# Kernel optimization log

Hardware: AMD Instinct MI355X
Metric: run time of the kernel (lower is better)

The kernel has to match this reference:

```python
import jax, jax.numpy as jnp
import numpy as np

NUM_ANTENNAS = 16
D = 0.5
WAVELENGTH = 1.0
RHO = 0.8


def setup_inputs() -> dict:
    key = jax.random.key(0)
    k = jax.random.split(key, 5)
    return {
        "W": jax.random.normal(k[0], (2_000_000, 2 * NUM_ANTENNAS), dtype=jnp.float32),
        "Hc_real": jax.random.normal(k[1], (4, 8, NUM_ANTENNAS), dtype=jnp.float32),
        "Hc_imag": jax.random.normal(k[2], (4, 8, NUM_ANTENNAS), dtype=jnp.float32),
        "Hs_real": jax.random.normal(k[3], (4, 4, NUM_ANTENNAS), dtype=jnp.float32),
        "Hs_imag": jax.random.normal(k[4], (4, 4, NUM_ANTENNAS), dtype=jnp.float32),
    }


def _estimate_angles(h_real, h_imag):
    """Vectorized version of the per-(b,t) phase-unwrap + OLS slope fit.

    h_real/h_imag: [B, T, N] -> angles [B, T] in degrees.
    """
    n = jnp.arange(NUM_ANTENNAS, dtype=h_real.dtype)
    phases = jnp.arctan2(h_imag, h_real)                      # torch.angle
    pd = jnp.diff(phases, axis=-1)
    pd = (pd + jnp.pi) % (2.0 * jnp.pi) - jnp.pi              # wrap to (-pi, pi]
    zeros = jnp.zeros(phases.shape[:-1] + (1,), phases.dtype)
    unwrapped = jnp.concatenate([zeros, jnp.cumsum(pd, axis=-1)], axis=-1)  # [B,T,N]
    # OLS slope of unwrapped vs n (closed form of solve(XtX, XtY) with X=[n,1])
    n_c = n - n.mean()
    slope = (unwrapped * n_c).sum(-1) / (n_c * n_c).sum()     # [B,T]
    sin_theta = jnp.clip(slope * WAVELENGTH / (2.0 * jnp.pi * D), -1.0, 1.0)
    return -jnp.rad2deg(jnp.arcsin(sin_theta))


def _steering_phase(angles_deg):
    # phase[t, n] = 2*pi*d*n*sin(theta_t)/wavelength  -> [T, N]
    n = jnp.arange(NUM_ANTENNAS, dtype=angles_deg.dtype)
    s = jnp.sin(jnp.deg2rad(angles_deg))
    return 2.0 * jnp.pi * D * s[:, None] * n[None, :] / WAVELENGTH


def reference(W, Hc_real, Hc_imag, Hs_real, Hs_imag):
    user_angles = _estimate_angles(Hc_real, Hc_imag)[0]       # [Tc]
    target_angles = _estimate_angles(Hs_real, Hs_imag)[0]     # [Ts]

    Wr = W[:, :NUM_ANTENNAS]
    Wi = W[:, NUM_ANTENNAS:]

    def gains(phase):  # |w_cplx @ conj(sv).T|, all-real math
        c = jnp.cos(phase)  # [T, N]
        s = jnp.sin(phase)
        re = Wr @ c.T + Wi @ s.T  # [B, T]
        im = Wi @ c.T - Wr @ s.T
        return jnp.sqrt(re * re + im * im)

    user_gains = gains(_steering_phase(user_angles))          # [B, Tc]
    target_gains = gains(_steering_phase(target_angles))      # [B, Ts]

    min_user_gain = user_gains.min(axis=1)
    sum_user_gain = user_gains.sum(axis=1)
    avg_target_gain = target_gains.mean(axis=1)

    comm_loss = -RHO * 2.5 * (min_user_gain + 0.1 * sum_user_gain)
    sens_loss = -(1.0 - RHO) * avg_target_gain
    return jnp.mean(comm_loss + sens_loss)
```

## Files before the change

### kernel.cpp

```cpp
#include <hip/hip_runtime.h>
#include <math.h>

#define NA 16
#define NBEAM 12
#define NUSER 8

#define ACC_OFFSET 1536

__global__ void mtl_angles_kernel(const float* __restrict__ Hc_r, const float* __restrict__ Hc_i,
                                  const float* __restrict__ Hs_r, const float* __restrict__ Hs_i,
                                  float* __restrict__ table, double* __restrict__ acc) {
    int t = threadIdx.x;
    if (t == 0) *acc = 0.0;
    if (t >= NBEAM) return;

    const float* re;
    const float* im;
    if (t < NUSER) { re = Hc_r + t * NA;           im = Hc_i + t * NA; }
    else           { re = Hs_r + (t - NUSER) * NA; im = Hs_i + (t - NUSER) * NA; }

    const float PI_F   = 3.14159265358979323846f;
    const float TWO_PI = 6.28318530717958647692f;

    float ph[NA];
    #pragma unroll
    for (int n = 0; n < NA; ++n) ph[n] = atan2f(im[n], re[n]);

    float unw = 0.f, dotsum = 0.f;
    #pragma unroll
    for (int n = 1; n < NA; ++n) {
        float pd = ph[n] - ph[n - 1];
        float x  = pd + PI_F;
        float m  = fmodf(x, TWO_PI);
        if (m < 0.f) m += TWO_PI;
        pd = m - PI_F;
        unw += pd;
        dotsum += unw * ((float)n - 7.5f);
    }
    float slope = dotsum / 340.0f;
    float sin_theta = slope / PI_F;
    sin_theta = fminf(1.0f, fmaxf(-1.0f, sin_theta));
    float st = -sin_theta;

    #pragma unroll
    for (int n = 0; n < NA; ++n) {
        float phase = PI_F * st * (float)n;
        table[t * 2 * NA + n]      = cosf(phase);
        table[t * 2 * NA + NA + n] = sinf(phase);
    }
}

__device__ __forceinline__ float dot4(float4 a, float4 b) {
    return a.x * b.x + a.y * b.y + a.z * b.z + a.w * b.w;
}

__global__ __launch_bounds__(256, 4) void mtl_gains_kernel(const float* __restrict__ W,
                                                           const float* __restrict__ table,
                                                           double* __restrict__ acc, int rows) {
    __shared__ float sh[NBEAM * 2 * NA];
    for (int i = threadIdx.x; i < NBEAM * 2 * NA; i += blockDim.x) sh[i] = table[i];
    __syncthreads();

    float local = 0.f;
    int tid = blockIdx.x * blockDim.x + threadIdx.x;
    int stride = gridDim.x * blockDim.x;
    #pragma unroll 1
    for (int row = tid; row < rows; row += stride) {
        const float4* wp = (const float4*)(W + (size_t)row * 32);
        float4 w[8];
        #pragma unroll
        for (int i = 0; i < 8; ++i) w[i] = wp[i];

        float minU = 3.4e38f, sumU = 0.f, sumT = 0.f;
        #pragma unroll 1
        for (int j = 0; j < NBEAM; ++j) {
            const float4* tc = (const float4*)(sh + j * 32);
            float re = 0.f, im = 0.f;
            #pragma unroll
            for (int q = 0; q < 4; ++q) {
                float4 c = tc[q], s = tc[q + 4];
                float4 wr = w[q], wi = w[q + 4];
                re += dot4(wr, c) + dot4(wi, s);
                im += dot4(wi, c) - dot4(wr, s);
            }
            float g = sqrtf(re * re + im * im);
            if (j < NUSER) { minU = fminf(minU, g); sumU += g; }
            else           { sumT += g; }
        }
        local += -2.0f * (minU + 0.1f * sumU) - 0.05f * sumT;
    }

    #pragma unroll
    for (int off = 32; off > 0; off >>= 1) local += __shfl_down(local, off);
    __shared__ float wsum[4];
    int lane = threadIdx.x & 63, wid = threadIdx.x >> 6;
    if (lane == 0) wsum[wid] = local;
    __syncthreads();
    if (threadIdx.x == 0) {
        float b = wsum[0] + wsum[1] + wsum[2] + wsum[3];
        atomicAdd(acc, (double)b);
    }
}

__global__ void mtl_finalize_kernel(const double* __restrict__ acc, float* __restrict__ out, int rows) {
    if (threadIdx.x == 0) out[0] = (float)(*acc / (double)rows);
}

extern "C" void kernel_launch(void* const* d_in, const int* in_sizes, int n_in,
                              void* d_out, int out_size, void* d_ws, size_t ws_size,
                              hipStream_t stream) {
    const float* W    = (const float*)d_in[0];
    const float* Hc_r = (const float*)d_in[1];
    const float* Hc_i = (const float*)d_in[2];
    const float* Hs_r = (const float*)d_in[3];
    const float* Hs_i = (const float*)d_in[4];
    float* out = (float*)d_out;

    int rows = in_sizes[0] / (2 * NA);
    float*  table = (float*)d_ws;
    double* acc   = (double*)((char*)d_ws + ACC_OFFSET);

    mtl_angles_kernel<<<1, 64, 0, stream>>>(Hc_r, Hc_i, Hs_r, Hs_i, table, acc);

    const int ROWS_PER_THREAD = 4;
    int blocks = (rows + 256 * ROWS_PER_THREAD - 1) / (256 * ROWS_PER_THREAD);
    mtl_gains_kernel<<<blocks, 256, 0, stream>>>(W, table, acc, rows);

    mtl_finalize_kernel<<<1, 64, 0, stream>>>(acc, out, rows);
}
```

Measured before the change: 366.4 us.

## Stage W tiles through LDS with direct global-to-LDS coalesced loads

Each block now loads a 256-row tile of W into shared memory using global_load_lds so that lanes issue contiguous 16-byte loads, then each thread reads its own row from LDS with a rotated index to spread bank accesses. The grid becomes up to 1024 persistent blocks looping over tiles, with a tail handled by block 0. This targets the strided per-thread row loads of the original, at the cost of two barriers per tile and no overlap between loading and computing.

```diff
diff --git a/kernel.cpp b/kernel.cpp
--- a/kernel.cpp
+++ b/kernel.cpp
@@ -54,45 +54,82 @@
     return a.x * b.x + a.y * b.y + a.z * b.z + a.w * b.w;
 }
 
+__device__ __forceinline__ void load_lds16(const float* g, float* l) {
+    __builtin_amdgcn_global_load_lds(
+        (const __attribute__((address_space(1))) void*)g,
+        (__attribute__((address_space(3))) void*)l, 16, 0, 0);
+}
+
+__device__ __forceinline__ float row_loss(const float4* w, const float* tbs) {
+    float minU = 3.4e38f, sumU = 0.f, sumT = 0.f;
+    #pragma unroll 1
+    for (int j = 0; j < NBEAM; ++j) {
+        const float4* tc = (const float4*)(tbs + j * 32);
+        float re = 0.f, im = 0.f;
+        #pragma unroll
+        for (int q = 0; q < 4; ++q) {
+            float4 c = tc[q], s = tc[q + 4];
+            float4 wr = w[q], wi = w[q + 4];
+            re += dot4(wr, c) + dot4(wi, s);
+            im += dot4(wi, c) - dot4(wr, s);
+        }
+        float g = sqrtf(re * re + im * im);
+        if (j < NUSER) { minU = fminf(minU, g); sumU += g; }
+        else           { sumT += g; }
+    }
+    return -2.0f * (minU + 0.1f * sumU) - 0.05f * sumT;
+}
+
 __global__ __launch_bounds__(256, 4) void mtl_gains_kernel(const float* __restrict__ W,
                                                            const float* __restrict__ table,
                                                            double* __restrict__ acc, int rows) {
-    __shared__ float sh[NBEAM * 2 * NA];
-    for (int i = threadIdx.x; i < NBEAM * 2 * NA; i += blockDim.x) sh[i] = table[i];
+    __shared__ float sh[256 * 32];
+    __shared__ float tbs[NBEAM * 2 * NA];
+    __shared__ float wsum[4];
+
+    for (int i = threadIdx.x; i < NBEAM * 2 * NA; i += blockDim.x) tbs[i] = table[i];
     __syncthreads();
 
+    const int t = threadIdx.x;
+    const int wave_base = (t & 192) * 4;
     float local = 0.f;
-    int tid = blockIdx.x * blockDim.x + threadIdx.x;
-    int stride = gridDim.x * blockDim.x;
+
+    const int ntiles = rows >> 8;
     #pragma unroll 1
-    for (int row = tid; row < rows; row += stride) {
-        const float4* wp = (const float4*)(W + (size_t)row * 32);
+    for (int tile = blockIdx.x; tile < ntiles; tile += gridDim.x) {
+        const float* gW = W + (size_t)tile * 256 * 32;
+        #pragma unroll
+        for (int i = 0; i < 8; ++i) {
+            int k = i * 256 + t;
+            load_lds16(gW + 4 * k, sh + i * 1024 + wave_base);
+        }
+        __syncthreads();
+
+        const float4* myrow = (const float4*)(sh + t * 32);
         float4 w[8];
         #pragma unroll
-        for (int i = 0; i < 8; ++i) w[i] = wp[i];
+        for (int i = 0; i < 8; ++i) {
+            int q = (t + i) & 7;
+            w[q] = myrow[q];
+        }
+        local += row_loss(w, tbs);
+        __syncthreads();
+    }
 
-        float minU = 3.4e38f, sumU = 0.f, sumT = 0.f;
-        #pragma unroll 1
-        for (int j = 0; j < NBEAM; ++j) {
-            const float4* tc = (const float4*)(sh + j * 32);
-            float re = 0.f, im = 0.f;
+    int tailbase = ntiles << 8;
+    if (blockIdx.x == 0) {
+        int row = tailbase + t;
+        if (row < rows) {
+            const float4* wp = (const float4*)(W + (size_t)row * 32);
+            float4 w[8];
             #pragma unroll
-            for (int q = 0; q < 4; ++q) {
-                float4 c = tc[q], s = tc[q + 4];
-                float4 wr = w[q], wi = w[q + 4];
-                re += dot4(wr, c) + dot4(wi, s);
-                im += dot4(wi, c) - dot4(wr, s);
-            }
-            float g = sqrtf(re * re + im * im);
-            if (j < NUSER) { minU = fminf(minU, g); sumU += g; }
-            else           { sumT += g; }
+            for (int i = 0; i < 8; ++i) w[i] = wp[i];
+            local += row_loss(w, tbs);
         }
-        local += -2.0f * (minU + 0.1f * sumU) - 0.05f * sumT;
     }
 
     #pragma unroll
     for (int off = 32; off > 0; off >>= 1) local += __shfl_down(local, off);
-    __shared__ float wsum[4];
     int lane = threadIdx.x & 63, wid = threadIdx.x >> 6;
     if (lane == 0) wsum[wid] = local;
     __syncthreads();
@@ -122,8 +159,8 @@
 
     mtl_angles_kernel<<<1, 64, 0, stream>>>(Hc_r, Hc_i, Hs_r, Hs_i, table, acc);
 
-    const int ROWS_PER_THREAD = 4;
-    int blocks = (rows + 256 * ROWS_PER_THREAD - 1) / (256 * ROWS_PER_THREAD);
+    int ntiles = rows >> 8;
+    int blocks = ntiles < 1024 ? (ntiles > 0 ? ntiles : 1) : 1024;
     mtl_gains_kernel<<<blocks, 256, 0, stream>>>(W, table, acc, rows);
 
     mtl_finalize_kernel<<<1, 64, 0, stream>>>(acc, out, rows);
```

Result: slower. 596.6 us (+62.8%).
